# Kernel tuning notes

Measured on AMD Instinct MI355X. Metric: run time of the kernel, lower is better.

Reference implementation:

```python
import math
import jax, jax.numpy as jnp
import numpy as np

B, LD, LS = 1, 512, 2048
C_S, C_H, H, PQ, PV = 384, 16, 12, 4, 8
EPS, INF = 1e-08, 1e9


def _quat_to_rot(q):
    q = q / jnp.linalg.norm(q, axis=-1, keepdims=True)
    w, x, y, z = q[..., 0], q[..., 1], q[..., 2], q[..., 3]
    R = jnp.stack([
        1 - 2 * (y * y + z * z), 2 * (x * y - w * z), 2 * (x * z + w * y),
        2 * (x * y + w * z), 1 - 2 * (x * x + z * z), 2 * (y * z - w * x),
        2 * (x * z - w * y), 2 * (y * z + w * x), 1 - 2 * (x * x + y * y)],
        axis=-1)
    return R.reshape(q.shape[:-1] + (3, 3))


def setup_inputs() -> dict:
    key = jax.random.key(0)
    ks = jax.random.split(key, 14)
    s_dst = jax.random.normal(ks[0], (B, LD, C_S), jnp.float32)
    s_src = jax.random.normal(ks[1], (B, LS, C_S), jnp.float32)
    R_dst = _quat_to_rot(jax.random.normal(ks[2], (B, LD, 4), jnp.float32))
    t_dst = jax.random.normal(ks[3], (B, LD, 3), jnp.float32) * 3.0
    R_src = _quat_to_rot(jax.random.normal(ks[4], (B, LS, 4), jnp.float32))
    t_src = jax.random.normal(ks[5], (B, LS, 3), jnp.float32) * 3.0
    dst_mask = jnp.ones((B, LD), jnp.float32)
    src_mask = (jax.random.uniform(ks[6], (B, LS)) < 0.9).astype(jnp.float32)
    sc = 0.02
    W_q = jax.random.normal(ks[7], (C_S, H * C_H), jnp.float32) * sc
    W_kv = jax.random.normal(ks[8], (C_S, 2 * H * C_H), jnp.float32) * sc
    W_qp = jax.random.normal(ks[9], (C_S, H * PQ * 3), jnp.float32) * sc
    W_kvp = jax.random.normal(ks[10], (C_S, H * (PQ + PV) * 3), jnp.float32) * sc
    W_out = jax.random.normal(ks[11], (H * (C_H + PV * 4), C_S), jnp.float32) * sc
    b_out = jnp.zeros((C_S,), jnp.float32)
    # ipa_point_weights_init_: softplus^-1(1) = log(e - 1)
    head_w = jnp.full((H,), float(np.log(np.e - 1.0)), jnp.float32)
    return dict(s_dst=s_dst, s_src=s_src, R_dst=R_dst, t_dst=t_dst,
                R_src=R_src, t_src=t_src, dst_mask=dst_mask, src_mask=src_mask,
                W_q=W_q, W_kv=W_kv, W_qp=W_qp, W_kvp=W_kvp,
                W_out=W_out, b_out=b_out, head_w=head_w)


def _split3_stack(x):
    # torch.split into 3 chunks on last dim then stack(dim=-1): [..., 3n] -> [..., n, 3]
    b, l, c3 = x.shape
    return jnp.moveaxis(x.reshape(b, l, 3, c3 // 3), -2, -1)


def _ipa_forward(s_dst, s_src, R_dst, t_dst, R_src, t_src, dst_mask, src_mask,
                 W_q, W_kv, W_qp, W_kvp, W_out, b_out, head_w):
    b, ld, _ = s_dst.shape
    ls = s_src.shape[1]
    gmask = (dst_mask[:, None, :, None] * src_mask[:, None, None, :])  # [B,1,Ld,Ls]

    q = (s_dst @ W_q).reshape(b, ld, H, C_H)
    kv = (s_src @ W_kv).reshape(b, ls, H, 2 * C_H)
    k, v = kv[..., :C_H], kv[..., C_H:]

    # points in global frame
    qp = _split3_stack(s_dst @ W_qp)                     # [B,Ld,H*PQ,3] local
    qp = jnp.einsum('blij,blpj->blpi', R_dst, qp) + t_dst[:, :, None, :]
    qp = qp.reshape(b, ld, H, PQ, 3)
    kvp = _split3_stack(s_src @ W_kvp)                   # [B,Ls,H*(PQ+PV),3]
    kvp = jnp.einsum('blij,blpj->blpi', R_src, kvp) + t_src[:, :, None, :]
    kvp = kvp.reshape(b, ls, H, PQ + PV, 3)
    k_pts, v_pts = kvp[..., :PQ, :], kvp[..., PQ:, :]

    # scalar attention scores
    a = jnp.einsum('bihc,bjhc->bhij', q, k) * math.sqrt(1.0 / (2 * C_H))
    a_sd = a * gmask

    # point attention: squared distances of global-frame points
    diff = qp[:, :, None, :, :, :] - k_pts[:, None, :, :, :, :]   # [B,Ld,Ls,H,PQ,3]
    pt2 = jnp.sum(diff * diff, axis=-1)                           # [B,Ld,Ls,H,PQ]
    hw = jax.nn.softplus(head_w) * math.sqrt(1.0 / (2 * (PQ * 9.0 / 2)))
    pt_att = jnp.sum(pt2 * hw[None, None, None, :, None], axis=-1) * (-0.5)
    pt_att = jnp.transpose(pt_att, (0, 3, 1, 2))                  # [B,H,Ld,Ls]
    a_pts = pt_att * gmask

    sq_mask = INF * (dst_mask[:, :, None] * src_mask[:, None, :] - 1.0)
    a = jax.nn.softmax(a + pt_att + sq_mask[:, None, :, :], axis=-1)

    # scalar value aggregation
    o = jnp.einsum('bhij,bjhc->bihc', a, v).reshape(b, ld, H * C_H)
    # point value aggregation, then back to dst local frame
    o_pt = jnp.einsum('bhij,bjhpc->bihpc', a, v_pts)              # [B,Ld,H,PV,3]
    o_pt = jnp.einsum('bikj,bihpk->bihpj', R_dst,
                      o_pt - t_dst[:, :, None, None, :])
    o_pt_norm = jnp.sqrt(jnp.sum(o_pt ** 2, axis=-1) + EPS).reshape(b, ld, H * PV)
    o_pt_flat = o_pt.reshape(b, ld, H * PV, 3)

    cat = jnp.concatenate([o, o_pt_flat[..., 0], o_pt_flat[..., 1],
                           o_pt_flat[..., 2], o_pt_norm], axis=-1)
    s_upd = cat @ W_out + b_out
    return s_upd, a, a_sd, a_pts


def reference(s_dst, s_src, R_dst, t_dst, R_src, t_src, dst_mask, src_mask,
              W_q, W_kv, W_qp, W_kvp, W_out, b_out, head_w):
    return _ipa_forward(s_dst, s_src, R_dst, t_dst, R_src, t_src,
                        dst_mask, src_mask, W_q, W_kv, W_qp, W_kvp,
                        W_out, b_out, head_w)
```

## Files before the change

### kernel.cpp

```cpp
#include <hip/hip_runtime.h>
#include <hip/hip_bf16.h>

#define LD 512
#define LS 2048
#define CS 384
#define CH 16
#define NH 12
#define PQ 4
#define PV 8
#define QCW 336
#define KVW 816

typedef __bf16 bf16x8 __attribute__((ext_vector_type(8)));
typedef float  f32x4  __attribute__((ext_vector_type(4)));

__device__ inline bf16x8 conv_frag(const float* __restrict__ p)
{
    float4 x = *(const float4*)p;
    float4 y = *(const float4*)(p + 4);
    bf16x8 h;
    h[0] = (__bf16)x.x; h[1] = (__bf16)x.y; h[2] = (__bf16)x.z; h[3] = (__bf16)x.w;
    h[4] = (__bf16)y.x; h[5] = (__bf16)y.y; h[6] = (__bf16)y.z; h[7] = (__bf16)y.w;
    return h;
}

__device__ inline bf16x8 conv_frag_w(const float* __restrict__ Wp, int stride)
{
    float f[8];
#pragma unroll
    for (int e = 0; e < 8; ++e) f[e] = Wp[(size_t)e * stride];
    bf16x8 h;
#pragma unroll
    for (int e = 0; e < 8; ++e) h[e] = (__bf16)f[e];
    return h;
}

__global__ __launch_bounds__(512) void proj_gemm_kernel(
    const float* __restrict__ s_dst, const float* __restrict__ s_src,
    const float* __restrict__ W_q, const float* __restrict__ W_qp,
    const float* __restrict__ W_kv, const float* __restrict__ W_kvp,
    float* __restrict__ qcat, float* __restrict__ kvcat)
{
    const float* A; float* C; int N, Nw, ncol0, n0, mbase; const float* Wsrc;
    if (blockIdx.x < 22) {
        int b = blockIdx.x;
        A = s_dst; C = qcat; N = QCW;
        int nt = b % 11, mg = b / 11;
        n0 = nt * 32; mbase = mg * 256;
        if (n0 < 192) { Wsrc = W_q;  Nw = 192; ncol0 = n0; }
        else          { Wsrc = W_qp; Nw = 144; ncol0 = n0 - 192; }
    } else {
        int b = blockIdx.x - 22;
        A = s_src; C = kvcat; N = KVW;
        int nt = b % 26, mg = b / 26;
        n0 = nt * 32; mbase = mg * 256;
        if (n0 < 384) { Wsrc = W_kv;  Nw = 384; ncol0 = n0; }
        else          { Wsrc = W_kvp; Nw = 432; ncol0 = n0 - 384; }
    }

    __shared__ float wlds[32][388];
    const int t = threadIdx.x;

#pragma unroll
    for (int s = 0; s < 24; ++s) {
        int idx = t + s * 512;
        int k = idx >> 5, c = idx & 31;
        float v = (ncol0 + c < Nw) ? Wsrc[(size_t)k * Nw + ncol0 + c] : 0.f;
        wlds[c][k] = v;
    }
    __syncthreads();

    const int lane = t & 63, wid = t >> 6;
    const int row16 = lane & 15, kq = lane >> 4;
    const int m0 = mbase + wid * 32;

    const float* ap0 = A + (size_t)(m0 + row16) * CS + kq * 8;
    const float* ap1 = ap0 + (size_t)16 * CS;
    const bool n1ok = (n0 + 16) < N;

    f32x4 acc00 = {0.f, 0.f, 0.f, 0.f};
    f32x4 acc10 = {0.f, 0.f, 0.f, 0.f};
    f32x4 acc01 = {0.f, 0.f, 0.f, 0.f};
    f32x4 acc11 = {0.f, 0.f, 0.f, 0.f};

#pragma unroll 4
    for (int k = 0; k < CS; k += 32) {
        bf16x8 a0 = conv_frag(ap0 + k);
        bf16x8 a1 = conv_frag(ap1 + k);
        bf16x8 b0 = conv_frag(&wlds[row16][k + kq * 8]);
        acc00 = __builtin_amdgcn_mfma_f32_16x16x32_bf16(a0, b0, acc00, 0, 0, 0);
        acc10 = __builtin_amdgcn_mfma_f32_16x16x32_bf16(a1, b0, acc10, 0, 0, 0);
        if (n1ok) {
            bf16x8 b1 = conv_frag(&wlds[row16 + 16][k + kq * 8]);
            acc01 = __builtin_amdgcn_mfma_f32_16x16x32_bf16(a0, b1, acc01, 0, 0, 0);
            acc11 = __builtin_amdgcn_mfma_f32_16x16x32_bf16(a1, b1, acc11, 0, 0, 0);
        }
    }

#pragma unroll
    for (int r = 0; r < 4; ++r) {
        const int mA = m0 + kq * 4 + r;
        const int mB = mA + 16;
        C[(size_t)mA * N + n0 + row16] = acc00[r];
        C[(size_t)mB * N + n0 + row16] = acc10[r];
        if (n1ok) {
            C[(size_t)mA * N + n0 + 16 + row16] = acc01[r];
            C[(size_t)mB * N + n0 + 16 + row16] = acc11[r];
        }
    }
}

__global__ __launch_bounds__(256) void prep_kernel(
    const float* __restrict__ qcat, const float* __restrict__ kvcat,
    const float* __restrict__ Rd, const float* __restrict__ td,
    const float* __restrict__ Rs, const float* __restrict__ ts,
    float* __restrict__ qp_rot, float* __restrict__ sqq,
    float* __restrict__ kT, float* __restrict__ vAllT,
    float* __restrict__ kpT, float* __restrict__ sqkT)
{
    const int t = threadIdx.x;
    if (blockIdx.y < NH) {
        const int h = blockIdx.y, j0 = blockIdx.x * 64;
        __shared__ float tile[64][33];
        __shared__ float ot[36][64];
        __shared__ float nrm[64][4];
        __shared__ float rt[64][12];

#pragma unroll
        for (int s = 0; s < 3; ++s) {
            int ld = t + s * 256;
            int jl = ld / 12, q = ld % 12;
            rt[jl][q] = (q < 9) ? Rs[(size_t)(j0 + jl) * 9 + q]
                                : ts[(size_t)(j0 + jl) * 3 + (q - 9)];
        }
#pragma unroll
        for (int r = 0; r < 2; ++r) {
            int f = t + r * 256;
            int jl = f >> 3, c4 = (f & 7) * 4;
            float4 v = *(const float4*)(kvcat + (size_t)(j0 + jl) * KVW + h * 32 + c4);
            tile[jl][c4 + 0] = v.x;
            tile[jl][c4 + 1] = v.y;
            tile[jl][c4 + 2] = v.z;
            tile[jl][c4 + 3] = v.w;
        }
        __syncthreads();

        {
            const int jl = t & 63, cr = t >> 6;
#pragma unroll
            for (int cg = 0; cg < 8; ++cg) {
                int c = cg * 4 + cr;
                float v = tile[jl][c];
                if (c < 16) kT[((size_t)h * 16 + c) * LS + j0 + jl] = v;
                else        vAllT[((size_t)h * 40 + (c - 16)) * LS + j0 + jl] = v;
            }
        }

#pragma unroll
        for (int s = 0; s < 3; ++s) {
            int u = t + s * 256;
            int jl = u / 12, p = u % 12;
            const float* src = kvcat + (size_t)(j0 + jl) * KVW + 384 + h * 12 + p;
            float x = src[0], y = src[144], z = src[288];
            const float* R = &rt[jl][0];
            float rx = R[0] * x + R[1] * y + R[2] * z + R[9];
            float ry = R[3] * x + R[4] * y + R[5] * z + R[10];
            float rz = R[6] * x + R[7] * y + R[8] * z + R[11];
            if (p < 4) {
                ot[p * 3 + 0][jl] = rx;
                ot[p * 3 + 1][jl] = ry;
                ot[p * 3 + 2][jl] = rz;
                nrm[jl][p] = rx * rx + ry * ry + rz * rz;
            } else {
                int r0 = 12 + (p - 4) * 3;
                ot[r0 + 0][jl] = rx;
                ot[r0 + 1][jl] = ry;
                ot[r0 + 2][jl] = rz;
            }
        }
        __syncthreads();

#pragma unroll
        for (int w = 0; w < 9; ++w) {
            int idx = t + w * 256;
            int row = idx >> 6, jl = idx & 63;
            float v = ot[row][jl];
            if (row < 12) kpT[((size_t)h * 12 + row) * LS + j0 + jl] = v;
            else          vAllT[((size_t)h * 40 + 16 + (row - 12)) * LS + j0 + jl] = v;
        }
        if (t < 64)
            sqkT[(size_t)h * LS + j0 + t] = nrm[t][0] + nrm[t][1] + nrm[t][2] + nrm[t][3];
    } else {
        const int i0 = blockIdx.x * 16;
        __shared__ float part[16][48];
        __shared__ float rtd[16][12];
        if (t < 192) {
            int il = t / 12, q = t % 12;
            rtd[il][q] = (q < 9) ? Rd[(size_t)(i0 + il) * 9 + q]
                                 : td[(size_t)(i0 + il) * 3 + (q - 9)];
        }
        __syncthreads();
#pragma unroll
        for (int s = 0; s < 3; ++s) {
            int u = t + s * 256;
            int il = u / 48, pt = u % 48;
            int i = i0 + il;
            float x = qcat[(size_t)i * QCW + 192 + pt];
            float y = qcat[(size_t)i * QCW + 240 + pt];
            float z = qcat[(size_t)i * QCW + 288 + pt];
            const float* R = &rtd[il][0];
            float rx = R[0] * x + R[1] * y + R[2] * z + R[9];
            float ry = R[3] * x + R[4] * y + R[5] * z + R[10];
            float rz = R[6] * x + R[7] * y + R[8] * z + R[11];
            qp_rot[(size_t)i * 144 + pt * 3 + 0] = rx;
            qp_rot[(size_t)i * 144 + pt * 3 + 1] = ry;
            qp_rot[(size_t)i * 144 + pt * 3 + 2] = rz;
            part[il][pt] = rx * rx + ry * ry + rz * rz;
        }
        __syncthreads();
        if (t < 192) {
            int il = t / 12, hh = t % 12;
            sqq[(size_t)(i0 + il) * NH + hh] =
                part[il][hh * 4] + part[il][hh * 4 + 1] +
                part[il][hh * 4 + 2] + part[il][hh * 4 + 3];
        }
    }
}

__global__ __launch_bounds__(256) void score_softmax_kernel(
    const float* __restrict__ qb, const float* __restrict__ kT,
    const float* __restrict__ qpb, const float* __restrict__ kpT,
    const float* __restrict__ sqq_g, const float* __restrict__ sqkT,
    const float* __restrict__ dmask, const float* __restrict__ smask,
    const float* __restrict__ head_w,
    float* __restrict__ a_out, float* __restrict__ asd_out,
    float* __restrict__ apts_out)
{
    const int h = blockIdx.y;
    const int i0 = blockIdx.x * 4;
    const int t = threadIdx.x;

    __shared__ float qs[4][32];
    __shared__ float sqq_s[4];
    __shared__ float dm_s[4];
    __shared__ float red[4][4];

    if (t < 128) {
        int i = t >> 5, c = t & 31;
        float v = 0.f;
        if (c < 16)      v = qb[(size_t)(i0 + i) * QCW + h * CH + c];
        else if (c < 28) v = qpb[(size_t)(i0 + i) * 144 + h * 12 + (c - 16)];
        qs[i][c] = v;
    } else if (t < 132) {
        int i = t - 128;
        sqq_s[i] = sqq_g[(size_t)(i0 + i) * NH + h];
        dm_s[i] = dmask[i0 + i];
    }
    const float hwv = log1pf(__expf(head_w[h])) * (1.0f / 6.0f);
    const float s1 = 0.17677669529663687f;
    const size_t rowbase = ((size_t)h * LD + i0) * LS;
    __syncthreads();

    float4 sregv[4][2];
    float mx[4] = {-3.0e38f, -3.0e38f, -3.0e38f, -3.0e38f};

#pragma unroll
    for (int jc = 0; jc < 2; ++jc) {
        const int j = (jc * 256 + t) * 4;
        float4 sm4 = *(const float4*)(smask + j);
        float4 sqk4 = *(const float4*)(sqkT + (size_t)h * LS + j);

        float4 kk[16];
#pragma unroll
        for (int c = 0; c < 16; ++c)
            kk[c] = *(const float4*)(kT + ((size_t)h * 16 + c) * LS + j);

        float4 qk4[4];
#pragma unroll
        for (int i = 0; i < 4; ++i) {
            const float4* q4 = (const float4*)&qs[i][0];
            float4 q0 = q4[0], q1 = q4[1], q2 = q4[2], q3 = q4[3];
            float4 a;
            a.x = q0.x * kk[0].x + q0.y * kk[1].x + q0.z * kk[2].x + q0.w * kk[3].x
                + q1.x * kk[4].x + q1.y * kk[5].x + q1.z * kk[6].x + q1.w * kk[7].x
                + q2.x * kk[8].x + q2.y * kk[9].x + q2.z * kk[10].x + q2.w * kk[11].x
                + q3.x * kk[12].x + q3.y * kk[13].x + q3.z * kk[14].x + q3.w * kk[15].x;
            a.y = q0.x * kk[0].y + q0.y * kk[1].y + q0.z * kk[2].y + q0.w * kk[3].y
                + q1.x * kk[4].y + q1.y * kk[5].y + q1.z * kk[6].y + q1.w * kk[7].y
                + q2.x * kk[8].y + q2.y * kk[9].y + q2.z * kk[10].y + q2.w * kk[11].y
                + q3.x * kk[12].y + q3.y * kk[13].y + q3.z * kk[14].y + q3.w * kk[15].y;
            a.z = q0.x * kk[0].z + q0.y * kk[1].z + q0.z * kk[2].z + q0.w * kk[3].z
                + q1.x * kk[4].z + q1.y * kk[5].z + q1.z * kk[6].z + q1.w * kk[7].z
                + q2.x * kk[8].z + q2.y * kk[9].z + q2.z * kk[10].z + q2.w * kk[11].z
                + q3.x * kk[12].z + q3.y * kk[13].z + q3.z * kk[14].z + q3.w * kk[15].z;
            a.w = q0.x * kk[0].w + q0.y * kk[1].w + q0.z * kk[2].w + q0.w * kk[3].w
                + q1.x * kk[4].w + q1.y * kk[5].w + q1.z * kk[6].w + q1.w * kk[7].w
                + q2.x * kk[8].w + q2.y * kk[9].w + q2.z * kk[10].w + q2.w * kk[11].w
                + q3.x * kk[12].w + q3.y * kk[13].w + q3.z * kk[14].w + q3.w * kk[15].w;
            qk4[i] = a;
        }

        float4 pp[12];
#pragma unroll
        for (int d = 0; d < 12; ++d)
            pp[d] = *(const float4*)(kpT + ((size_t)h * 12 + d) * LS + j);

        float4 dp4[4];
#pragma unroll
        for (int i = 0; i < 4; ++i) {
            const float4* r4 = (const float4*)&qs[i][16];
            float4 r0 = r4[0], r1 = r4[1], r2 = r4[2];
            float4 d;
            d.x = r0.x * pp[0].x + r0.y * pp[1].x + r0.z * pp[2].x + r0.w * pp[3].x
                + r1.x * pp[4].x + r1.y * pp[5].x + r1.z * pp[6].x + r1.w * pp[7].x
                + r2.x * pp[8].x + r2.y * pp[9].x + r2.z * pp[10].x + r2.w * pp[11].x;
            d.y = r0.x * pp[0].y + r0.y * pp[1].y + r0.z * pp[2].y + r0.w * pp[3].y
                + r1.x * pp[4].y + r1.y * pp[5].y + r1.z * pp[6].y + r1.w * pp[7].y
                + r2.x * pp[8].y + r2.y * pp[9].y + r2.z * pp[10].y + r2.w * pp[11].y;
            d.z = r0.x * pp[0].z + r0.y * pp[1].z + r0.z * pp[2].z + r0.w * pp[3].z
                + r1.x * pp[4].z + r1.y * pp[5].z + r1.z * pp[6].z + r1.w * pp[7].z
                + r2.x * pp[8].z + r2.y * pp[9].z + r2.z * pp[10].z + r2.w * pp[11].z;
            d.w = r0.x * pp[0].w + r0.y * pp[1].w + r0.z * pp[2].w + r0.w * pp[3].w
                + r1.x * pp[4].w + r1.y * pp[5].w + r1.z * pp[6].w + r1.w * pp[7].w
                + r2.x * pp[8].w + r2.y * pp[9].w + r2.z * pp[10].w + r2.w * pp[11].w;
            dp4[i] = d;
        }

#pragma unroll
        for (int i = 0; i < 4; ++i) {
            float sqq = sqq_s[i];
            float dm = dm_s[i];
            float4 qk, pt, g, logit;
            qk.x = qk4[i].x * s1; qk.y = qk4[i].y * s1;
            qk.z = qk4[i].z * s1; qk.w = qk4[i].w * s1;
            pt.x = -0.5f * hwv * (sqq + sqk4.x - 2.f * dp4[i].x);
            pt.y = -0.5f * hwv * (sqq + sqk4.y - 2.f * dp4[i].y);
            pt.z = -0.5f * hwv * (sqq + sqk4.z - 2.f * dp4[i].z);
            pt.w = -0.5f * hwv * (sqq + sqk4.w - 2.f * dp4[i].w);
            g.x = dm * sm4.x; g.y = dm * sm4.y; g.z = dm * sm4.z; g.w = dm * sm4.w;
            size_t idx = rowbase + (size_t)i * LS + j;
            f32x4 asd = {qk.x * g.x, qk.y * g.y, qk.z * g.z, qk.w * g.w};
            f32x4 apts = {pt.x * g.x, pt.y * g.y, pt.z * g.z, pt.w * g.w};
            __builtin_nontemporal_store(asd, (f32x4*)(asd_out + idx));
            __builtin_nontemporal_store(apts, (f32x4*)(apts_out + idx));
            logit.x = qk.x + pt.x + 1.0e9f * (g.x - 1.0f);
            logit.y = qk.y + pt.y + 1.0e9f * (g.y - 1.0f);
            logit.z = qk.z + pt.z + 1.0e9f * (g.z - 1.0f);
            logit.w = qk.w + pt.w + 1.0e9f * (g.w - 1.0f);
            sregv[i][jc] = logit;
            mx[i] = fmaxf(mx[i], fmaxf(fmaxf(logit.x, logit.y), fmaxf(logit.z, logit.w)));
        }
    }

    const int lane = t & 63, wid = t >> 6;
#pragma unroll
    for (int i = 0; i < 4; ++i) {
        float v = mx[i];
        for (int off = 32; off > 0; off >>= 1) v = fmaxf(v, __shfl_xor(v, off));
        if (lane == 0) red[wid][i] = v;
    }
    __syncthreads();
    float M[4], sum[4] = {0.f, 0.f, 0.f, 0.f};
#pragma unroll
    for (int i = 0; i < 4; ++i)
        M[i] = fmaxf(fmaxf(red[0][i], red[1][i]), fmaxf(red[2][i], red[3][i]));
    __syncthreads();

#pragma unroll
    for (int jc = 0; jc < 2; ++jc) {
#pragma unroll
        for (int i = 0; i < 4; ++i) {
            float4 e;
            e.x = __expf(sregv[i][jc].x - M[i]);
            e.y = __expf(sregv[i][jc].y - M[i]);
            e.z = __expf(sregv[i][jc].z - M[i]);
            e.w = __expf(sregv[i][jc].w - M[i]);
            sregv[i][jc] = e;
            sum[i] += e.x + e.y + e.z + e.w;
        }
    }
#pragma unroll
    for (int i = 0; i < 4; ++i) {
        float v = sum[i];
        for (int off = 32; off > 0; off >>= 1) v += __shfl_xor(v, off);
        if (lane == 0) red[wid][i] = v;
    }
    __syncthreads();
    float inv[4];
#pragma unroll
    for (int i = 0; i < 4; ++i)
        inv[i] = 1.0f / (red[0][i] + red[1][i] + red[2][i] + red[3][i]);

#pragma unroll
    for (int jc = 0; jc < 2; ++jc) {
        const int j = (jc * 256 + t) * 4;
#pragma unroll
        for (int i = 0; i < 4; ++i) {
            float4 e = sregv[i][jc];
            float4 o = make_float4(e.x * inv[i], e.y * inv[i], e.z * inv[i], e.w * inv[i]);
            *(float4*)(a_out + rowbase + (size_t)i * LS + j) = o;
        }
    }
}

__global__ __launch_bounds__(512) void av_mfma_kernel(
    const float* __restrict__ a, const float* __restrict__ vAllT,
    float* __restrict__ o_buf, float* __restrict__ opt_buf)
{
    const int m0 = blockIdx.x * 16;
    const int h  = blockIdx.y;
    const int t = threadIdx.x;
    const int lane = t & 63;
    const int wid  = t >> 6;
    const int row16 = lane & 15, kq = lane >> 4;

    const size_t kbase = (size_t)wid * 256 + kq * 8;
    const float* ap  = a     + ((size_t)h * LD + m0 + row16) * LS + kbase;
    const float* v0p = vAllT + ((size_t)h * 40 +  0 + row16) * LS + kbase;
    const float* v1p = vAllT + ((size_t)h * 40 + 16 + row16) * LS + kbase;
    const float* v2p = vAllT + ((size_t)h * 40 + 24 + row16) * LS + kbase;

    f32x4 acc0 = {0.f, 0.f, 0.f, 0.f};
    f32x4 acc1 = {0.f, 0.f, 0.f, 0.f};
    f32x4 acc2 = {0.f, 0.f, 0.f, 0.f};

#pragma unroll 2
    for (int kk = 0; kk < 256; kk += 32) {
        bf16x8 ah = conv_frag(ap + kk);
        bf16x8 b0 = conv_frag(v0p + kk);
        bf16x8 b1 = conv_frag(v1p + kk);
        bf16x8 b2 = conv_frag(v2p + kk);
        acc0 = __builtin_amdgcn_mfma_f32_16x16x32_bf16(ah, b0, acc0, 0, 0, 0);
        acc1 = __builtin_amdgcn_mfma_f32_16x16x32_bf16(ah, b1, acc1, 0, 0, 0);
        acc2 = __builtin_amdgcn_mfma_f32_16x16x32_bf16(ah, b2, acc2, 0, 0, 0);
    }

    __shared__ float red[8][64][13];
#pragma unroll
    for (int r = 0; r < 4; ++r) {
        red[wid][lane][r]     = acc0[r];
        red[wid][lane][4 + r] = acc1[r];
        red[wid][lane][8 + r] = acc2[r];
    }
    __syncthreads();

    if (wid == 0) {
        float s[12];
#pragma unroll
        for (int r = 0; r < 12; ++r) {
            float v = red[0][lane][r];
#pragma unroll
            for (int w = 1; w < 8; ++w) v += red[w][lane][r];
            s[r] = v;
        }
        const int ib = m0 + kq * 4;
#pragma unroll
        for (int r = 0; r < 4; ++r) {
            const int i = ib + r;
            o_buf[(size_t)i * 192 + h * 16 + row16] = s[r];
            opt_buf[(size_t)i * 288 + h * 24 + row16] = s[4 + r];
            if (row16 >= 8)
                opt_buf[(size_t)i * 288 + h * 24 + 8 + row16] = s[8 + r];
        }
    }
}

__global__ __launch_bounds__(64) void finalize_out_kernel(
    const float* __restrict__ o_buf, const float* __restrict__ opt_buf,
    const float* __restrict__ Rd, const float* __restrict__ td,
    const float* __restrict__ W_out, const float* __restrict__ bias,
    float* __restrict__ out_s)
{
    const int m0 = blockIdx.x * 16;
    const int n0 = blockIdx.y * 32;
    const int t = threadIdx.x;

    __shared__ float cat[16][596];

    for (int u = t; u < 16 * 192; u += 64) {
        int il = u / 192, c = u % 192;
        cat[il][c] = o_buf[(size_t)(m0 + il) * 192 + c];
    }
    for (int u = t; u < 16 * 96; u += 64) {
        int il = u / 96, p = u % 96;
        int i = m0 + il;
        const float* op = opt_buf + (size_t)i * 288 + p * 3;
        float x = op[0] - td[i * 3 + 0];
        float y = op[1] - td[i * 3 + 1];
        float z = op[2] - td[i * 3 + 2];
        const float* R = Rd + i * 9;
        float rx = R[0] * x + R[3] * y + R[6] * z;
        float ry = R[1] * x + R[4] * y + R[7] * z;
        float rz = R[2] * x + R[5] * y + R[8] * z;
        cat[il][192 + p] = rx;
        cat[il][288 + p] = ry;
        cat[il][384 + p] = rz;
        cat[il][480 + p] = sqrtf(rx * rx + ry * ry + rz * rz + 1e-8f);
    }
    __syncthreads();

    const int row16 = t & 15, kq = t >> 4;
    f32x4 acc0 = {0.f, 0.f, 0.f, 0.f};
    f32x4 acc1 = {0.f, 0.f, 0.f, 0.f};

    for (int k = 0; k < 576; k += 32) {
        bf16x8 af = conv_frag(&cat[row16][k + kq * 8]);
        bf16x8 b0 = conv_frag_w(W_out + (size_t)(k + kq * 8) * CS + n0 + row16, CS);
        bf16x8 b1 = conv_frag_w(W_out + (size_t)(k + kq * 8) * CS + n0 + 16 + row16, CS);
        acc0 = __builtin_amdgcn_mfma_f32_16x16x32_bf16(af, b0, acc0, 0, 0, 0);
        acc1 = __builtin_amdgcn_mfma_f32_16x16x32_bf16(af, b1, acc1, 0, 0, 0);
    }

    const float bv0 = bias[n0 + row16];
    const float bv1 = bias[n0 + 16 + row16];
#pragma unroll
    for (int r = 0; r < 4; ++r) {
        const int m = m0 + kq * 4 + r;
        out_s[(size_t)m * CS + n0 + row16] = acc0[r] + bv0;
        out_s[(size_t)m * CS + n0 + 16 + row16] = acc1[r] + bv1;
    }
}

extern "C" void kernel_launch(void* const* d_in, const int* in_sizes, int n_in,
                              void* d_out, int out_size, void* d_ws, size_t ws_size,
                              hipStream_t stream)
{
    (void)in_sizes; (void)n_in; (void)out_size; (void)ws_size;
    const float* s_dst    = (const float*)d_in[0];
    const float* s_src    = (const float*)d_in[1];
    const float* R_dst    = (const float*)d_in[2];
    const float* t_dst    = (const float*)d_in[3];
    const float* R_src    = (const float*)d_in[4];
    const float* t_src    = (const float*)d_in[5];
    const float* dst_mask = (const float*)d_in[6];
    const float* src_mask = (const float*)d_in[7];
    const float* W_q      = (const float*)d_in[8];
    const float* W_kv     = (const float*)d_in[9];
    const float* W_qp     = (const float*)d_in[10];
    const float* W_kvp    = (const float*)d_in[11];
    const float* W_out    = (const float*)d_in[12];
    const float* b_out    = (const float*)d_in[13];
    const float* head_w   = (const float*)d_in[14];

    float* ws = (float*)d_ws;
    float* qcat    = ws;
    float* kvcat   = qcat    + 172032;
    float* qp_rot  = kvcat   + 1671168;
    float* sq_q    = qp_rot  + 73728;
    float* o_buf   = sq_q    + 6144;
    float* opt_buf = o_buf   + 98304;
    float* kT      = opt_buf + 147456;
    float* vAllT   = kT      + 393216;
    float* kpT     = vAllT   + 983040;
    float* sqkT    = kpT     + 294912;

    float* out_s    = (float*)d_out;
    float* out_a    = out_s    + 196608;
    float* out_asd  = out_a    + 12582912;
    float* out_apts = out_asd  + 12582912;

    proj_gemm_kernel<<<dim3(230), dim3(512), 0, stream>>>(
        s_dst, s_src, W_q, W_qp, W_kv, W_kvp, qcat, kvcat);
    prep_kernel<<<dim3(32, 13), dim3(256), 0, stream>>>(
        qcat, kvcat, R_dst, t_dst, R_src, t_src,
        qp_rot, sq_q, kT, vAllT, kpT, sqkT);
    score_softmax_kernel<<<dim3(LD / 4, NH), dim3(256), 0, stream>>>(
        qcat, kT, qp_rot, kpT, sq_q, sqkT, dst_mask, src_mask, head_w,
        out_a, out_asd, out_apts);
    av_mfma_kernel<<<dim3(LD / 16, NH), dim3(512), 0, stream>>>(out_a, vAllT, o_buf, opt_buf);
    finalize_out_kernel<<<dim3(32, 12), dim3(64), 0, stream>>>(
        o_buf, opt_buf, R_dst, t_dst, W_out, b_out, out_s);
}
```

Baseline: 273.7 us.

## Fuse score/softmax kernel with attention-value MFMA kernel into one launch

Merges the score+softmax kernel and the attention-times-value MFMA kernel into a single kernel. Each block now handles 16 destination rows by looping over four groups of four rows for the softmax. It then runs the AV product over the freshly written attention rows, with four waves each covering 512 source positions. This removes one kernel launch and aims to re-read the attention matrix while it is still hot in cache. In exchange, the grid shrinks fourfold, which lowers parallelism and serialises the softmax work within each block.

After: 388.6 us. +42.0%, slower.

```diff
diff --git a/kernel.cpp b/kernel.cpp
--- a/kernel.cpp
+++ b/kernel.cpp
@@ -227,240 +227,238 @@
     }
 }
 
-__global__ __launch_bounds__(256) void score_softmax_kernel(
+__global__ __launch_bounds__(256) void score_av_kernel(
     const float* __restrict__ qb, const float* __restrict__ kT,
     const float* __restrict__ qpb, const float* __restrict__ kpT,
     const float* __restrict__ sqq_g, const float* __restrict__ sqkT,
     const float* __restrict__ dmask, const float* __restrict__ smask,
-    const float* __restrict__ head_w,
+    const float* __restrict__ head_w, const float* __restrict__ vAllT,
     float* __restrict__ a_out, float* __restrict__ asd_out,
-    float* __restrict__ apts_out)
+    float* __restrict__ apts_out,
+    float* __restrict__ o_buf, float* __restrict__ opt_buf)
 {
     const int h = blockIdx.y;
-    const int i0 = blockIdx.x * 4;
+    const int m0 = blockIdx.x * 16;
     const int t = threadIdx.x;
+    const int lane = t & 63, wid = t >> 6;
+    const int row16 = lane & 15, kq = lane >> 4;
 
     __shared__ float qs[4][32];
     __shared__ float sqq_s[4];
     __shared__ float dm_s[4];
     __shared__ float red[4][4];
-
-    if (t < 128) {
-        int i = t >> 5, c = t & 31;
-        float v = 0.f;
-        if (c < 16)      v = qb[(size_t)(i0 + i) * QCW + h * CH + c];
-        else if (c < 28) v = qpb[(size_t)(i0 + i) * 144 + h * 12 + (c - 16)];
-        qs[i][c] = v;
-    } else if (t < 132) {
-        int i = t - 128;
-        sqq_s[i] = sqq_g[(size_t)(i0 + i) * NH + h];
-        dm_s[i] = dmask[i0 + i];
-    }
+    __shared__ float redav[4][64][13];
+
     const float hwv = log1pf(__expf(head_w[h])) * (1.0f / 6.0f);
     const float s1 = 0.17677669529663687f;
-    const size_t rowbase = ((size_t)h * LD + i0) * LS;
+
+    for (int g = 0; g < 4; ++g) {
+        const int i0 = m0 + g * 4;
+        __syncthreads();
+        if (t < 128) {
+            int i = t >> 5, c = t & 31;
+            float v = 0.f;
+            if (c < 16)      v = qb[(size_t)(i0 + i) * QCW + h * CH + c];
+            else if (c < 28) v = qpb[(size_t)(i0 + i) * 144 + h * 12 + (c - 16)];
+            qs[i][c] = v;
+        } else if (t < 132) {
+            int i = t - 128;
+            sqq_s[i] = sqq_g[(size_t)(i0 + i) * NH + h];
+            dm_s[i] = dmask[i0 + i];
+        }
+        const size_t rowbase = ((size_t)h * LD + i0) * LS;
+        __syncthreads();
+
+        float4 sregv[4][2];
+        float mx[4] = {-3.0e38f, -3.0e38f, -3.0e38f, -3.0e38f};
+
+#pragma unroll
+        for (int jc = 0; jc < 2; ++jc) {
+            const int j = (jc * 256 + t) * 4;
+            float4 sm4 = *(const float4*)(smask + j);
+            float4 sqk4 = *(const float4*)(sqkT + (size_t)h * LS + j);
+
+            float4 kk[16];
+#pragma unroll
+            for (int c = 0; c < 16; ++c)
+                kk[c] = *(const float4*)(kT + ((size_t)h * 16 + c) * LS + j);
+
+            float4 qk4[4];
+#pragma unroll
+            for (int i = 0; i < 4; ++i) {
+                const float4* q4 = (const float4*)&qs[i][0];
+                float4 q0 = q4[0], q1 = q4[1], q2 = q4[2], q3 = q4[3];
+                float4 a;
+                a.x = q0.x * kk[0].x + q0.y * kk[1].x + q0.z * kk[2].x + q0.w * kk[3].x
+                    + q1.x * kk[4].x + q1.y * kk[5].x + q1.z * kk[6].x + q1.w * kk[7].x
+                    + q2.x * kk[8].x + q2.y * kk[9].x + q2.z * kk[10].x + q2.w * kk[11].x
+                    + q3.x * kk[12].x + q3.y * kk[13].x + q3.z * kk[14].x + q3.w * kk[15].x;
+                a.y = q0.x * kk[0].y + q0.y * kk[1].y + q0.z * kk[2].y + q0.w * kk[3].y
+                    + q1.x * kk[4].y + q1.y * kk[5].y + q1.z * kk[6].y + q1.w * kk[7].y
+                    + q2.x * kk[8].y + q2.y * kk[9].y + q2.z * kk[10].y + q2.w * kk[11].y
+                    + q3.x * kk[12].y + q3.y * kk[13].y + q3.z * kk[14].y + q3.w * kk[15].y;
+                a.z = q0.x * kk[0].z + q0.y * kk[1].z + q0.z * kk[2].z + q0.w * kk[3].z
+                    + q1.x * kk[4].z + q1.y * kk[5].z + q1.z * kk[6].z + q1.w * kk[7].z
+                    + q2.x * kk[8].z + q2.y * kk[9].z + q2.z * kk[10].z + q2.w * kk[11].z
+                    + q3.x * kk[12].z + q3.y * kk[13].z + q3.z * kk[14].z + q3.w * kk[15].z;
+                a.w = q0.x * kk[0].w + q0.y * kk[1].w + q0.z * kk[2].w + q0.w * kk[3].w
+                    + q1.x * kk[4].w + q1.y * kk[5].w + q1.z * kk[6].w + q1.w * kk[7].w
+                    + q2.x * kk[8].w + q2.y * kk[9].w + q2.z * kk[10].w + q2.w * kk[11].w
+                    + q3.x * kk[12].w + q3.y * kk[13].w + q3.z * kk[14].w + q3.w * kk[15].w;
+                qk4[i] = a;
+            }
+
+            float4 pp[12];
+#pragma unroll
+            for (int d = 0; d < 12; ++d)
+                pp[d] = *(const float4*)(kpT + ((size_t)h * 12 + d) * LS + j);
+
+            float4 dp4[4];
+#pragma unroll
+            for (int i = 0; i < 4; ++i) {
+                const float4* r4 = (const float4*)&qs[i][16];
+                float4 r0 = r4[0], r1 = r4[1], r2 = r4[2];
+                float4 d;
+                d.x = r0.x * pp[0].x + r0.y * pp[1].x + r0.z * pp[2].x + r0.w * pp[3].x
+                    + r1.x * pp[4].x + r1.y * pp[5].x + r1.z * pp[6].x + r1.w * pp[7].x
+                    + r2.x * pp[8].x + r2.y * pp[9].x + r2.z * pp[10].x + r2.w * pp[11].x;
+                d.y = r0.x * pp[0].y + r0.y * pp[1].y + r0.z * pp[2].y + r0.w * pp[3].y
+                    + r1.x * pp[4].y + r1.y * pp[5].y + r1.z * pp[6].y + r1.w * pp[7].y
+                    + r2.x * pp[8].y + r2.y * pp[9].y + r2.z * pp[10].y + r2.w * pp[11].y;
+                d.z = r0.x * pp[0].z + r0.y * pp[1].z + r0.z * pp[2].z + r0.w * pp[3].z
+                    + r1.x * pp[4].z + r1.y * pp[5].z + r1.z * pp[6].z + r1.w * pp[7].z
+                    + r2.x * pp[8].z + r2.y * pp[9].z + r2.z * pp[10].z + r2.w * pp[11].z;
+                d.w = r0.x * pp[0].w + r0.y * pp[1].w + r0.z * pp[2].w + r0.w * pp[3].w
+                    + r1.x * pp[4].w + r1.y * pp[5].w + r1.z * pp[6].w + r1.w * pp[7].w
+                    + r2.x * pp[8].w + r2.y * pp[9].w + r2.z * pp[10].w + r2.w * pp[11].w;
+                dp4[i] = d;
+            }
+
+#pragma unroll
+            for (int i = 0; i < 4; ++i) {
+                float sqq = sqq_s[i];
+                float dm = dm_s[i];
+                float4 qk, pt, g4, logit;
+                qk.x = qk4[i].x * s1; qk.y = qk4[i].y * s1;
+                qk.z = qk4[i].z * s1; qk.w = qk4[i].w * s1;
+                pt.x = -0.5f * hwv * (sqq + sqk4.x - 2.f * dp4[i].x);
+                pt.y = -0.5f * hwv * (sqq + sqk4.y - 2.f * dp4[i].y);
+                pt.z = -0.5f * hwv * (sqq + sqk4.z - 2.f * dp4[i].z);
+                pt.w = -0.5f * hwv * (sqq + sqk4.w - 2.f * dp4[i].w);
+                g4.x = dm * sm4.x; g4.y = dm * sm4.y; g4.z = dm * sm4.z; g4.w = dm * sm4.w;
+                size_t idx = rowbase + (size_t)i * LS + j;
+                f32x4 asd = {qk.x * g4.x, qk.y * g4.y, qk.z * g4.z, qk.w * g4.w};
+                f32x4 apts = {pt.x * g4.x, pt.y * g4.y, pt.z * g4.z, pt.w * g4.w};
+                __builtin_nontemporal_store(asd, (f32x4*)(asd_out + idx));
+                __builtin_nontemporal_store(apts, (f32x4*)(apts_out + idx));
+                logit.x = qk.x + pt.x + 1.0e9f * (g4.x - 1.0f);
+                logit.y = qk.y + pt.y + 1.0e9f * (g4.y - 1.0f);
+                logit.z = qk.z + pt.z + 1.0e9f * (g4.z - 1.0f);
+                logit.w = qk.w + pt.w + 1.0e9f * (g4.w - 1.0f);
+                sregv[i][jc] = logit;
+                mx[i] = fmaxf(mx[i], fmaxf(fmaxf(logit.x, logit.y), fmaxf(logit.z, logit.w)));
+            }
+        }
+
+#pragma unroll
+        for (int i = 0; i < 4; ++i) {
+            float v = mx[i];
+            for (int off = 32; off > 0; off >>= 1) v = fmaxf(v, __shfl_xor(v, off));
+            if (lane == 0) red[wid][i] = v;
+        }
+        __syncthreads();
+        float M[4], sum[4] = {0.f, 0.f, 0.f, 0.f};
+#pragma unroll
+        for (int i = 0; i < 4; ++i)
+            M[i] = fmaxf(fmaxf(red[0][i], red[1][i]), fmaxf(red[2][i], red[3][i]));
+        __syncthreads();
+
+#pragma unroll
+        for (int jc = 0; jc < 2; ++jc) {
+#pragma unroll
+            for (int i = 0; i < 4; ++i) {
+                float4 e;
+                e.x = __expf(sregv[i][jc].x - M[i]);
+                e.y = __expf(sregv[i][jc].y - M[i]);
+                e.z = __expf(sregv[i][jc].z - M[i]);
+                e.w = __expf(sregv[i][jc].w - M[i]);
+                sregv[i][jc] = e;
+                sum[i] += e.x + e.y + e.z + e.w;
+            }
+        }
+#pragma unroll
+        for (int i = 0; i < 4; ++i) {
+            float v = sum[i];
+            for (int off = 32; off > 0; off >>= 1) v += __shfl_xor(v, off);
+            if (lane == 0) red[wid][i] = v;
+        }
+        __syncthreads();
+        float inv[4];
+#pragma unroll
+        for (int i = 0; i < 4; ++i)
+            inv[i] = 1.0f / (red[0][i] + red[1][i] + red[2][i] + red[3][i]);
+
+#pragma unroll
+        for (int jc = 0; jc < 2; ++jc) {
+            const int j = (jc * 256 + t) * 4;
+#pragma unroll
+            for (int i = 0; i < 4; ++i) {
+                float4 e = sregv[i][jc];
+                float4 o = make_float4(e.x * inv[i], e.y * inv[i], e.z * inv[i], e.w * inv[i]);
+                *(float4*)(a_out + rowbase + (size_t)i * LS + j) = o;
+            }
+        }
+    }
+
     __syncthreads();
-
-    float4 sregv[4][2];
-    float mx[4] = {-3.0e38f, -3.0e38f, -3.0e38f, -3.0e38f};
-
-#pragma unroll
-    for (int jc = 0; jc < 2; ++jc) {
-        const int j = (jc * 256 + t) * 4;
-        float4 sm4 = *(const float4*)(smask + j);
-        float4 sqk4 = *(const float4*)(sqkT + (size_t)h * LS + j);
-
-        float4 kk[16];
-#pragma unroll
-        for (int c = 0; c < 16; ++c)
-            kk[c] = *(const float4*)(kT + ((size_t)h * 16 + c) * LS + j);
-
-        float4 qk4[4];
-#pragma unroll
-        for (int i = 0; i < 4; ++i) {
-            const float4* q4 = (const float4*)&qs[i][0];
-            float4 q0 = q4[0], q1 = q4[1], q2 = q4[2], q3 = q4[3];
-            float4 a;
-            a.x = q0.x * kk[0].x + q0.y * kk[1].x + q0.z * kk[2].x + q0.w * kk[3].x
-                + q1.x * kk[4].x + q1.y * kk[5].x + q1.z * kk[6].x + q1.w * kk[7].x
-                + q2.x * kk[8].x + q2.y * kk[9].x + q2.z * kk[10].x + q2.w * kk[11].x
-                + q3.x * kk[12].x + q3.y * kk[13].x + q3.z * kk[14].x + q3.w * kk[15].x;
-            a.y = q0.x * kk[0].y + q0.y * kk[1].y + q0.z * kk[2].y + q0.w * kk[3].y
-                + q1.x * kk[4].y + q1.y * kk[5].y + q1.z * kk[6].y + q1.w * kk[7].y
-                + q2.x * kk[8].y + q2.y * kk[9].y + q2.z * kk[10].y + q2.w * kk[11].y
-                + q3.x * kk[12].y + q3.y * kk[13].y + q3.z * kk[14].y + q3.w * kk[15].y;
-            a.z = q0.x * kk[0].z + q0.y * kk[1].z + q0.z * kk[2].z + q0.w * kk[3].z
-                + q1.x * kk[4].z + q1.y * kk[5].z + q1.z * kk[6].z + q1.w * kk[7].z
-                + q2.x * kk[8].z + q2.y * kk[9].z + q2.z * kk[10].z + q2.w * kk[11].z
-                + q3.x * kk[12].z + q3.y * kk[13].z + q3.z * kk[14].z + q3.w * kk[15].z;
-            a.w = q0.x * kk[0].w + q0.y * kk[1].w + q0.z * kk[2].w + q0.w * kk[3].w
-                + q1.x * kk[4].w + q1.y * kk[5].w + q1.z * kk[6].w + q1.w * kk[7].w
-                + q2.x * kk[8].w + q2.y * kk[9].w + q2.z * kk[10].w + q2.w * kk[11].w
-                + q3.x * kk[12].w + q3.y * kk[13].w + q3.z * kk[14].w + q3.w * kk[15].w;
-            qk4[i] = a;
-        }
-
-        float4 pp[12];
-#pragma unroll
-        for (int d = 0; d < 12; ++d)
-            pp[d] = *(const float4*)(kpT + ((size_t)h * 12 + d) * LS + j);
-
-        float4 dp4[4];
-#pragma unroll
-        for (int i = 0; i < 4; ++i) {
-            const float4* r4 = (const float4*)&qs[i][16];
-            float4 r0 = r4[0], r1 = r4[1], r2 = r4[2];
-            float4 d;
-            d.x = r0.x * pp[0].x + r0.y * pp[1].x + r0.z * pp[2].x + r0.w * pp[3].x
-                + r1.x * pp[4].x + r1.y * pp[5].x + r1.z * pp[6].x + r1.w * pp[7].x
-                + r2.x * pp[8].x + r2.y * pp[9].x + r2.z * pp[10].x + r2.w * pp[11].x;
-            d.y = r0.x * pp[0].y + r0.y * pp[1].y + r0.z * pp[2].y + r0.w * pp[3].y
-                + r1.x * pp[4].y + r1.y * pp[5].y + r1.z * pp[6].y + r1.w * pp[7].y
-                + r2.x * pp[8].y + r2.y * pp[9].y + r2.z * pp[10].y + r2.w * pp[11].y;
-            d.z = r0.x * pp[0].z + r0.y * pp[1].z + r0.z * pp[2].z + r0.w * pp[3].z
-                + r1.x * pp[4].z + r1.y * pp[5].z + r1.z * pp[6].z + r1.w * pp[7].z
-                + r2.x * pp[8].z + r2.y * pp[9].z + r2.z * pp[10].z + r2.w * pp[11].z;
-            d.w = r0.x * pp[0].w + r0.y * pp[1].w + r0.z * pp[2].w + r0.w * pp[3].w
-                + r1.x * pp[4].w + r1.y * pp[5].w + r1.z * pp[6].w + r1.w * pp[7].w
-                + r2.x * pp[8].w + r2.y * pp[9].w + r2.z * pp[10].w + r2.w * pp[11].w;
-            dp4[i] = d;
-        }
-
-#pragma unroll
-        for (int i = 0; i < 4; ++i) {
-            float sqq = sqq_s[i];
-            float dm = dm_s[i];
-            float4 qk, pt, g, logit;
-            qk.x = qk4[i].x * s1; qk.y = qk4[i].y * s1;
-            qk.z = qk4[i].z * s1; qk.w = qk4[i].w * s1;
-            pt.x = -0.5f * hwv * (sqq + sqk4.x - 2.f * dp4[i].x);
-            pt.y = -0.5f * hwv * (sqq + sqk4.y - 2.f * dp4[i].y);
-            pt.z = -0.5f * hwv * (sqq + sqk4.z - 2.f * dp4[i].z);
-            pt.w = -0.5f * hwv * (sqq + sqk4.w - 2.f * dp4[i].w);
-            g.x = dm * sm4.x; g.y = dm * sm4.y; g.z = dm * sm4.z; g.w = dm * sm4.w;
-            size_t idx = rowbase + (size_t)i * LS + j;
-            f32x4 asd = {qk.x * g.x, qk.y * g.y, qk.z * g.z, qk.w * g.w};
-            f32x4 apts = {pt.x * g.x, pt.y * g.y, pt.z * g.z, pt.w * g.w};
-            __builtin_nontemporal_store(asd, (f32x4*)(asd_out + idx));
-            __builtin_nontemporal_store(apts, (f32x4*)(apts_out + idx));
-            logit.x = qk.x + pt.x + 1.0e9f * (g.x - 1.0f);
-            logit.y = qk.y + pt.y + 1.0e9f * (g.y - 1.0f);
-            logit.z = qk.z + pt.z + 1.0e9f * (g.z - 1.0f);
-            logit.w = qk.w + pt.w + 1.0e9f * (g.w - 1.0f);
-            sregv[i][jc] = logit;
-            mx[i] = fmaxf(mx[i], fmaxf(fmaxf(logit.x, logit.y), fmaxf(logit.z, logit.w)));
-        }
-    }
-
-    const int lane = t & 63, wid = t >> 6;
-#pragma unroll
-    for (int i = 0; i < 4; ++i) {
-        float v = mx[i];
-        for (int off = 32; off > 0; off >>= 1) v = fmaxf(v, __shfl_xor(v, off));
-        if (lane == 0) red[wid][i] = v;
-    }
-    __syncthreads();
-    float M[4], sum[4] = {0.f, 0.f, 0.f, 0.f};
-#pragma unroll
-    for (int i = 0; i < 4; ++i)
-        M[i] = fmaxf(fmaxf(red[0][i], red[1][i]), fmaxf(red[2][i], red[3][i]));
-    __syncthreads();
-
-#pragma unroll
-    for (int jc = 0; jc < 2; ++jc) {
-#pragma unroll
-        for (int i = 0; i < 4; ++i) {
-            float4 e;
-            e.x = __expf(sregv[i][jc].x - M[i]);
-            e.y = __expf(sregv[i][jc].y - M[i]);
-            e.z = __expf(sregv[i][jc].z - M[i]);
-            e.w = __expf(sregv[i][jc].w - M[i]);
-            sregv[i][jc] = e;
-            sum[i] += e.x + e.y + e.z + e.w;
-        }
-    }
-#pragma unroll
-    for (int i = 0; i < 4; ++i) {
-        float v = sum[i];
-        for (int off = 32; off > 0; off >>= 1) v += __shfl_xor(v, off);
-        if (lane == 0) red[wid][i] = v;
-    }
-    __syncthreads();
-    float inv[4];
-#pragma unroll
-    for (int i = 0; i < 4; ++i)
-        inv[i] = 1.0f / (red[0][i] + red[1][i] + red[2][i] + red[3][i]);
-
-#pragma unroll
-    for (int jc = 0; jc < 2; ++jc) {
-        const int j = (jc * 256 + t) * 4;
-#pragma unroll
-        for (int i = 0; i < 4; ++i) {
-            float4 e = sregv[i][jc];
-            float4 o = make_float4(e.x * inv[i], e.y * inv[i], e.z * inv[i], e.w * inv[i]);
-            *(float4*)(a_out + rowbase + (size_t)i * LS + j) = o;
-        }
-    }
-}
-
-__global__ __launch_bounds__(512) void av_mfma_kernel(
-    const float* __restrict__ a, const float* __restrict__ vAllT,
-    float* __restrict__ o_buf, float* __restrict__ opt_buf)
-{
-    const int m0 = blockIdx.x * 16;
-    const int h  = blockIdx.y;
-    const int t = threadIdx.x;
-    const int lane = t & 63;
-    const int wid  = t >> 6;
-    const int row16 = lane & 15, kq = lane >> 4;
-
-    const size_t kbase = (size_t)wid * 256 + kq * 8;
-    const float* ap  = a     + ((size_t)h * LD + m0 + row16) * LS + kbase;
-    const float* v0p = vAllT + ((size_t)h * 40 +  0 + row16) * LS + kbase;
-    const float* v1p = vAllT + ((size_t)h * 40 + 16 + row16) * LS + kbase;
-    const float* v2p = vAllT + ((size_t)h * 40 + 24 + row16) * LS + kbase;
-
-    f32x4 acc0 = {0.f, 0.f, 0.f, 0.f};
-    f32x4 acc1 = {0.f, 0.f, 0.f, 0.f};
-    f32x4 acc2 = {0.f, 0.f, 0.f, 0.f};
+    {
+        const size_t kbase = (size_t)wid * 512 + kq * 8;
+        const float* ap  = a_out + ((size_t)h * LD + m0 + row16) * LS + kbase;
+        const float* v0p = vAllT + ((size_t)h * 40 +  0 + row16) * LS + kbase;
+        const float* v1p = vAllT + ((size_t)h * 40 + 16 + row16) * LS + kbase;
+        const float* v2p = vAllT + ((size_t)h * 40 + 24 + row16) * LS + kbase;
+
+        f32x4 acc0 = {0.f, 0.f, 0.f, 0.f};
+        f32x4 acc1 = {0.f, 0.f, 0.f, 0.f};
+        f32x4 acc2 = {0.f, 0.f, 0.f, 0.f};
 
 #pragma unroll 2
-    for (int kk = 0; kk < 256; kk += 32) {
-        bf16x8 ah = conv_frag(ap + kk);
-        bf16x8 b0 = conv_frag(v0p + kk);
-        bf16x8 b1 = conv_frag(v1p + kk);
-        bf16x8 b2 = conv_frag(v2p + kk);
-        acc0 = __builtin_amdgcn_mfma_f32_16x16x32_bf16(ah, b0, acc0, 0, 0, 0);
-        acc1 = __builtin_amdgcn_mfma_f32_16x16x32_bf16(ah, b1, acc1, 0, 0, 0);
-        acc2 = __builtin_amdgcn_mfma_f32_16x16x32_bf16(ah, b2, acc2, 0, 0, 0);
-    }
-
-    __shared__ float red[8][64][13];
-#pragma unroll
-    for (int r = 0; r < 4; ++r) {
-        red[wid][lane][r]     = acc0[r];
-        red[wid][lane][4 + r] = acc1[r];
-        red[wid][lane][8 + r] = acc2[r];
-    }
-    __syncthreads();
-
-    if (wid == 0) {
-        float s[12];
-#pragma unroll
-        for (int r = 0; r < 12; ++r) {
-            float v = red[0][lane][r];
-#pragma unroll
-            for (int w = 1; w < 8; ++w) v += red[w][lane][r];
-            s[r] = v;
-        }
-        const int ib = m0 + kq * 4;
+        for (int kk = 0; kk < 512; kk += 32) {
+            bf16x8 ah = conv_frag(ap + kk);
+            bf16x8 b0 = conv_frag(v0p + kk);
+            bf16x8 b1 = conv_frag(v1p + kk);
+            bf16x8 b2 = conv_frag(v2p + kk);
+            acc0 = __builtin_amdgcn_mfma_f32_16x16x32_bf16(ah, b0, acc0, 0, 0, 0);
+            acc1 = __builtin_amdgcn_mfma_f32_16x16x32_bf16(ah, b1, acc1, 0, 0, 0);
+            acc2 = __builtin_amdgcn_mfma_f32_16x16x32_bf16(ah, b2, acc2, 0, 0, 0);
+        }
+
 #pragma unroll
         for (int r = 0; r < 4; ++r) {
-            const int i = ib + r;
-            o_buf[(size_t)i * 192 + h * 16 + row16] = s[r];
-            opt_buf[(size_t)i * 288 + h * 24 + row16] = s[4 + r];
-            if (row16 >= 8)
-                opt_buf[(size_t)i * 288 + h * 24 + 8 + row16] = s[8 + r];
+            redav[wid][lane][r]     = acc0[r];
+            redav[wid][lane][4 + r] = acc1[r];
+            redav[wid][lane][8 + r] = acc2[r];
+        }
+        __syncthreads();
+
+        if (wid == 0) {
+            float s[12];
+#pragma unroll
+            for (int r = 0; r < 12; ++r) {
+                float v = redav[0][lane][r];
+#pragma unroll
+                for (int w = 1; w < 4; ++w) v += redav[w][lane][r];
+                s[r] = v;
+            }
+            const int ib = m0 + kq * 4;
+#pragma unroll
+            for (int r = 0; r < 4; ++r) {
+                const int i = ib + r;
+                o_buf[(size_t)i * 192 + h * 16 + row16] = s[r];
+                opt_buf[(size_t)i * 288 + h * 24 + row16] = s[4 + r];
+                if (row16 >= 8)
+                    opt_buf[(size_t)i * 288 + h * 24 + 8 + row16] = s[8 + r];
+            }
         }
     }
 }
@@ -564,10 +562,9 @@
     prep_kernel<<<dim3(32, 13), dim3(256), 0, stream>>>(
         qcat, kvcat, R_dst, t_dst, R_src, t_src,
         qp_rot, sq_q, kT, vAllT, kpT, sqkT);
-    score_softmax_kernel<<<dim3(LD / 4, NH), dim3(256), 0, stream>>>(
-        qcat, kT, qp_rot, kpT, sq_q, sqkT, dst_mask, src_mask, head_w,
-        out_a, out_asd, out_apts);
-    av_mfma_kernel<<<dim3(LD / 16, NH), dim3(512), 0, stream>>>(out_a, vAllT, o_buf, opt_buf);
+    score_av_kernel<<<dim3(LD / 16, NH), dim3(256), 0, stream>>>(
+        qcat, kT, qp_rot, kpT, sq_q, sqkT, dst_mask, src_mask, head_w, vAllT,
+        out_a, out_asd, out_apts, o_buf, opt_buf);
     finalize_out_kernel<<<dim3(32, 12), dim3(64), 0, stream>>>(
         o_buf, opt_buf, R_dst, t_dst, W_out, b_out, out_s);
 }
```
